# Performance work log

Measured on AMD Instinct MI355X. Metric: run time of the kernel, lower is better.

Reference implementation:

```python
import jax, jax.numpy as jnp
import numpy as np

B, T, D = 2, 1024, 1024
V = 50257
K = 20  # n_noise_samples


def setup_inputs() -> dict:
    key = jax.random.key(0)
    k1, k2, k3, k4 = jax.random.split(key, 4)
    hidden = jax.random.normal(k1, (B, T, D), dtype=jnp.float32)
    targets = jax.random.randint(k2, (B, T), 0, V, dtype=jnp.int32)
    W = jax.random.normal(k3, (V, D), dtype=jnp.float32) * 0.02  # output_proj weight (V, D)
    noise_ids = jax.random.randint(k4, (K,), 0, V, dtype=jnp.int32)
    return {"hidden": hidden, "targets": targets, "W": W, "noise_ids": noise_ids}


def reference(hidden, targets, W, noise_ids):
    b, t, d = hidden.shape
    n = b * t
    h = hidden.reshape(n, d)            # (N, D)
    tgt = targets.reshape(n)            # (N,)
    # full-vocab projection, as in nn.Linear(d_model, vocab, bias=False)
    logits = h @ W.T                    # (N, V); temperature == 1.0 -> no-op
    scores_pos = logits[jnp.arange(n), tgt]                 # (N,)
    scores_neg = logits[:, noise_ids].reshape(-1)           # (N*K,)
    k = noise_ids.shape[0]
    log_k = jnp.log(jnp.float32(k))
    log_unif = -jnp.log(jnp.float32(W.shape[0]))            # sampler is None -> uniform noise
    pos_terms = jax.nn.log_sigmoid(scores_pos - log_k - log_unif)
    neg_terms = jax.nn.log_sigmoid(-(scores_neg - log_k - log_unif))
    loss = -pos_terms.mean() - neg_terms.mean()
    return loss
```

## Files before the change

kernel.cpp:

```cpp
#include <hip/hip_runtime.h>
#include <cmath>


#define KN 20

__device__ __forceinline__ float log_sigmoid_f(float x) {
    return fminf(x, 0.0f) - log1pf(expf(-fabsf(x)));
}

__device__ __forceinline__ float fma4(float4 a, float4 b, float acc) {
    acc = fmaf(a.x, b.x, acc);
    acc = fmaf(a.y, b.y, acc);
    acc = fmaf(a.z, b.z, acc);
    return fmaf(a.w, b.w, acc);
}

__device__ __forceinline__ float wave_reduce(float v) {
    #pragma unroll
    for (int off = 32; off > 0; off >>= 1) v += __shfl_xor(v, off, 64);
    return v;
}

__global__ __launch_bounds__(256) void nce_rows_kernel(
    const float* __restrict__ hidden,
    const int*   __restrict__ targets,
    const float* __restrict__ W,
    const int*   __restrict__ noise_ids,
    float* __restrict__ cb4,
    float inv_n, float inv_nk, float shift)
{
    const int row  = blockIdx.x;
    const int tid  = threadIdx.x;
    const int wave = tid >> 6;
    const int lane = tid & 63;

    const float* hrow = hidden + (size_t)row * 1024;
    float4 h[4];
    #pragma unroll
    for (int j = 0; j < 4; ++j)
        h[j] = *reinterpret_cast<const float4*>(hrow + lane * 4 + j * 256);

    const int tgt = targets[row];

    float acc[6];
    #pragma unroll
    for (int s = 0; s < 6; ++s) {
        const int id = wave + 4 * s;
        float a = 0.0f;
        if (id <= KN) {
            const int wrow = (id == 0) ? tgt : noise_ids[id - 1];
            const float* wr = W + (size_t)wrow * 1024;
            #pragma unroll
            for (int j = 0; j < 4; ++j) {
                const float4 b = *reinterpret_cast<const float4*>(wr + lane * 4 + j * 256);
                a = fma4(h[j], b, a);
            }
        }
        acc[s] = a;
    }

    #pragma unroll
    for (int off = 32; off > 0; off >>= 1)
        #pragma unroll
        for (int s = 0; s < 6; ++s)
            acc[s] += __shfl_xor(acc[s], off, 64);

    float v = acc[0];
    v = (lane == 1) ? acc[1] : v;
    v = (lane == 2) ? acc[2] : v;
    v = (lane == 3) ? acc[3] : v;
    v = (lane == 4) ? acc[4] : v;
    v = (lane == 5) ? acc[5] : v;
    const int id = wave + 4 * lane;
    float term = 0.0f;
    if (lane < 6 && id <= KN) {
        const float sc = v + shift;
        term = (id == 0) ? (-log_sigmoid_f(sc)) * inv_n
                         : (-log_sigmoid_f(-sc)) * inv_nk;
    }
    term += __shfl_xor(term, 1, 64);
    term += __shfl_xor(term, 2, 64);
    term += __shfl_xor(term, 4, 64);

    if (lane == 0) cb4[row * 4 + wave] = term;
}

__global__ __launch_bounds__(256) void nce_generic_kernel(
    const float* __restrict__ hidden, const int* __restrict__ targets,
    const float* __restrict__ W, const int* __restrict__ noise_ids,
    float* __restrict__ cb4, int D, int K, float inv_n, float inv_nk, float shift)
{
    const int row  = blockIdx.x;
    const int tid  = threadIdx.x;
    const int wave = tid >> 6;
    const int lane = tid & 63;

    const float* hrow = hidden + (size_t)row * D;
    const int tgt = targets[row];
    float c = 0.0f;
    for (int id = wave; id <= K; id += 4) {
        const int wrow = (id == 0) ? tgt : noise_ids[id - 1];
        const float* wv = W + (size_t)wrow * D;
        float acc = 0.0f;
        for (int k = lane; k < D; k += 64) acc = fmaf(hrow[k], wv[k], acc);
        acc = wave_reduce(acc);
        if (lane == 0) {
            const float s = acc + shift;
            c += (id == 0) ? (-log_sigmoid_f(s)) * inv_n
                           : (-log_sigmoid_f(-s)) * inv_nk;
        }
    }
    if (lane == 0) cb4[row * 4 + wave] = c;
}

__global__ __launch_bounds__(256) void nce_sum_kernel(
    const float* __restrict__ cb4, float* __restrict__ out, int n4)
{
    __shared__ float sp[4];
    const int tid  = threadIdx.x;
    const int wave = tid >> 6;
    const int lane = tid & 63;

    const float4* v = reinterpret_cast<const float4*>(cb4);
    const int nv = n4 >> 2;
    float p = 0.0f;
    for (int i = tid; i < nv; i += 256) {
        const float4 x = v[i];
        p += (x.x + x.y) + (x.z + x.w);
    }
    p = wave_reduce(p);
    if (lane == 0) sp[wave] = p;
    __syncthreads();
    if (tid == 0) out[0] = sp[0] + sp[1] + sp[2] + sp[3];
}

extern "C" void kernel_launch(void* const* d_in, const int* in_sizes, int n_in,
                              void* d_out, int out_size, void* d_ws, size_t ws_size,
                              hipStream_t stream) {
    const float* hidden    = (const float*)d_in[0];
    const int*   targets   = (const int*)d_in[1];
    const float* W         = (const float*)d_in[2];
    const int*   noise_ids = (const int*)d_in[3];

    const int N = in_sizes[1];
    const int D = in_sizes[0] / N;
    const int K = in_sizes[3];
    const int V = in_sizes[2] / D;

    const float shift  = logf((float)V) - logf((float)K);
    const float inv_n  = 1.0f / (float)N;
    const float inv_nk = 1.0f / ((float)N * (float)K);

    float* cb4 = (float*)d_ws;

    if (D == 1024 && K == KN) {
        nce_rows_kernel<<<N, 256, 0, stream>>>(
            hidden, targets, W, noise_ids, cb4, inv_n, inv_nk, shift);
    } else {
        nce_generic_kernel<<<N, 256, 0, stream>>>(
            hidden, targets, W, noise_ids, cb4, D, K, inv_n, inv_nk, shift);
    }
    nce_sum_kernel<<<1, 256, 0, stream>>>(cb4, (float*)d_out, 4 * N);
}
```

Baseline: 17.81 us.

## Process two rows per block so each noise W row load serves both rows

The row kernel now handles two hidden rows per 512-thread block. Both rows are staged in shared memory, and each wave computes dot products of a noise W row against both hidden rows, which halves the number of W-row fetches per output row. The target dot products are assigned to two spare waves. In exchange it adds an LDS staging step and a barrier, and it halves the grid size. This could reduce latency hiding, and the two waves doing only target work leave some load imbalance.

```diff
diff --git a/kernel.cpp b/kernel.cpp
--- a/kernel.cpp
+++ b/kernel.cpp
@@ -21,68 +21,98 @@
     return v;
 }
 
-__global__ __launch_bounds__(256) void nce_rows_kernel(
+__global__ __launch_bounds__(512) void nce_rows2_kernel(
     const float* __restrict__ hidden,
     const int*   __restrict__ targets,
     const float* __restrict__ W,
     const int*   __restrict__ noise_ids,
-    float* __restrict__ cb4,
+    float* __restrict__ cbw,
     float inv_n, float inv_nk, float shift)
 {
-    const int row  = blockIdx.x;
+    __shared__ float hlds[2048];
+
     const int tid  = threadIdx.x;
     const int wave = tid >> 6;
     const int lane = tid & 63;
+    const int r0   = blockIdx.x * 2;
 
-    const float* hrow = hidden + (size_t)row * 1024;
-    float4 h[4];
+    reinterpret_cast<float4*>(hlds)[tid] =
+        reinterpret_cast<const float4*>(hidden + (size_t)r0 * 1024)[tid];
+
+    const int tgt0 = targets[r0];
+    const int tgt1 = targets[r0 + 1];
+    __syncthreads();
+
+    float acc[3][2];
     #pragma unroll
-    for (int j = 0; j < 4; ++j)
-        h[j] = *reinterpret_cast<const float4*>(hrow + lane * 4 + j * 256);
+    for (int s = 0; s < 3; ++s) { acc[s][0] = 0.0f; acc[s][1] = 0.0f; }
 
-    const int tgt = targets[row];
+    #pragma unroll
+    for (int s = 0; s < 2; ++s) {
+        const int n = wave + 8 * s;
+        const float* wr = W + (size_t)noise_ids[n] * 1024;
+        #pragma unroll
+        for (int j = 0; j < 4; ++j) {
+            const float4 b  = *reinterpret_cast<const float4*>(wr + lane * 4 + j * 256);
+            const float4 a0 = *reinterpret_cast<const float4*>(hlds + lane * 4 + j * 256);
+            const float4 a1 = *reinterpret_cast<const float4*>(hlds + 1024 + lane * 4 + j * 256);
+            acc[s][0] = fma4(b, a0, acc[s][0]);
+            acc[s][1] = fma4(b, a1, acc[s][1]);
+        }
+    }
 
-    float acc[6];
-    #pragma unroll
-    for (int s = 0; s < 6; ++s) {
-        const int id = wave + 4 * s;
-        float a = 0.0f;
-        if (id <= KN) {
-            const int wrow = (id == 0) ? tgt : noise_ids[id - 1];
-            const float* wr = W + (size_t)wrow * 1024;
-            #pragma unroll
-            for (int j = 0; j < 4; ++j) {
-                const float4 b = *reinterpret_cast<const float4*>(wr + lane * 4 + j * 256);
-                a = fma4(h[j], b, a);
-            }
+    if (wave < 4) {
+        const float* wr = W + (size_t)noise_ids[16 + wave] * 1024;
+        #pragma unroll
+        for (int j = 0; j < 4; ++j) {
+            const float4 b  = *reinterpret_cast<const float4*>(wr + lane * 4 + j * 256);
+            const float4 a0 = *reinterpret_cast<const float4*>(hlds + lane * 4 + j * 256);
+            const float4 a1 = *reinterpret_cast<const float4*>(hlds + 1024 + lane * 4 + j * 256);
+            acc[2][0] = fma4(b, a0, acc[2][0]);
+            acc[2][1] = fma4(b, a1, acc[2][1]);
         }
-        acc[s] = a;
+    } else if (wave < 6) {
+        const int r = wave - 4;
+        const float* wr = W + (size_t)(r == 0 ? tgt0 : tgt1) * 1024;
+        const float* hr = hlds + r * 1024;
+        #pragma unroll
+        for (int j = 0; j < 4; ++j) {
+            const float4 b = *reinterpret_cast<const float4*>(wr + lane * 4 + j * 256);
+            const float4 a = *reinterpret_cast<const float4*>(hr + lane * 4 + j * 256);
+            acc[2][0] = fma4(b, a, acc[2][0]);
+        }
     }
 
     #pragma unroll
     for (int off = 32; off > 0; off >>= 1)
         #pragma unroll
-        for (int s = 0; s < 6; ++s)
-            acc[s] += __shfl_xor(acc[s], off, 64);
+        for (int s = 0; s < 3; ++s) {
+            acc[s][0] += __shfl_xor(acc[s][0], off, 64);
+            acc[s][1] += __shfl_xor(acc[s][1], off, 64);
+        }
 
-    float v = acc[0];
-    v = (lane == 1) ? acc[1] : v;
-    v = (lane == 2) ? acc[2] : v;
-    v = (lane == 3) ? acc[3] : v;
-    v = (lane == 4) ? acc[4] : v;
-    v = (lane == 5) ? acc[5] : v;
-    const int id = wave + 4 * lane;
+    float v = acc[0][0];
+    v = (lane == 1) ? acc[0][1] : v;
+    v = (lane == 2) ? acc[1][0] : v;
+    v = (lane == 3) ? acc[1][1] : v;
+    v = (lane == 4) ? acc[2][0] : v;
+    v = (lane == 5) ? acc[2][1] : v;
+
     float term = 0.0f;
-    if (lane < 6 && id <= KN) {
-        const float sc = v + shift;
-        term = (id == 0) ? (-log_sigmoid_f(sc)) * inv_n
-                         : (-log_sigmoid_f(-sc)) * inv_nk;
+    if (lane < 6) {
+        const bool valid  = (lane < 4) || (wave < 4) || (lane == 4 && wave < 6);
+        const bool is_pos = (lane == 4 && wave >= 4);
+        if (valid) {
+            const float sc = v + shift;
+            term = is_pos ? (-log_sigmoid_f(sc)) * inv_n
+                          : (-log_sigmoid_f(-sc)) * inv_nk;
+        }
     }
     term += __shfl_xor(term, 1, 64);
     term += __shfl_xor(term, 2, 64);
     term += __shfl_xor(term, 4, 64);
 
-    if (lane == 0) cb4[row * 4 + wave] = term;
+    if (lane == 0) cbw[blockIdx.x * 8 + wave] = term;
 }
 
 __global__ __launch_bounds__(256) void nce_generic_kernel(
@@ -114,14 +144,14 @@
 }
 
 __global__ __launch_bounds__(256) void nce_sum_kernel(
-    const float* __restrict__ cb4, float* __restrict__ out, int n4)
+    const float* __restrict__ cbw, float* __restrict__ out, int n4)
 {
     __shared__ float sp[4];
     const int tid  = threadIdx.x;
     const int wave = tid >> 6;
     const int lane = tid & 63;
 
-    const float4* v = reinterpret_cast<const float4*>(cb4);
+    const float4* v = reinterpret_cast<const float4*>(cbw);
     const int nv = n4 >> 2;
     float p = 0.0f;
     for (int i = tid; i < nv; i += 256) {
@@ -151,14 +181,14 @@
     const float inv_n  = 1.0f / (float)N;
     const float inv_nk = 1.0f / ((float)N * (float)K);
 
-    float* cb4 = (float*)d_ws;
+    float* cbw = (float*)d_ws;
 
-    if (D == 1024 && K == KN) {
-        nce_rows_kernel<<<N, 256, 0, stream>>>(
-            hidden, targets, W, noise_ids, cb4, inv_n, inv_nk, shift);
+    if (D == 1024 && K == KN && (N % 2) == 0) {
+        nce_rows2_kernel<<<N / 2, 512, 0, stream>>>(
+            hidden, targets, W, noise_ids, cbw, inv_n, inv_nk, shift);
     } else {
         nce_generic_kernel<<<N, 256, 0, stream>>>(
-            hidden, targets, W, noise_ids, cb4, D, K, inv_n, inv_nk, shift);
+            hidden, targets, W, noise_ids, cbw, D, K, inv_n, inv_nk, shift);
     }
-    nce_sum_kernel<<<1, 256, 0, stream>>>(cb4, (float*)d_out, 4 * N);
+    nce_sum_kernel<<<1, 256, 0, stream>>>(cbw, (float*)d_out, 4 * N);
 }
```

Result: faster. 16.47 us, median of 2 (-7.5%).
